# Performance work log

Hardware: AMD Instinct MI355X
Metric: run time of the kernel (lower is better)

Reference implementation:

```python
import jax, jax.numpy as jnp
import numpy as np


def _t2p(x):
    # [B, N, C] -> [B, C, H, H]
    B, N, C = x.shape
    H = int(round(N ** 0.5))
    return x.transpose(0, 2, 1).reshape(B, C, H, H)


def _p2t(x):
    # [B, C, H, W] -> [B, H*W, C]
    B, C, H, W = x.shape
    return x.reshape(B, C, H * W).transpose(0, 2, 1)


def _ln(x, g, b, eps=1e-5):
    m = jnp.mean(x, axis=-1, keepdims=True)
    v = jnp.var(x, axis=-1, keepdims=True)
    return (x - m) / jnp.sqrt(v + eps) * g + b


def _spectral(x, cw):
    # x: [B, C, H, W]; cw: [h, w//2+1, C, 2]
    y = x.transpose(0, 3, 2, 1).astype(jnp.float32)  # [B, W, H, C]
    a, b = y.shape[1], y.shape[2]
    f = jnp.fft.rfft2(y, axes=(1, 2), norm='ortho')   # [B, a, b//2+1, C]
    w = cw[..., 0] + 1j * cw[..., 1]
    y = jnp.fft.irfft2(f * w, s=(a, b), axes=(1, 2), norm='ortho')
    return y.transpose(0, 3, 2, 1)                    # [B, C, H, W]


def _branch(tok, cw, ln1_g, ln1_b, ln2_g, ln2_b, W1, b1, W2, b2):
    # tok: [B, N, 8]
    raw = tok
    t1 = _ln(_p2t(_t2p(tok)), ln1_g, ln1_b)
    p1 = _spectral(_t2p(t1), cw)
    t2 = _ln(_p2t(p1), ln2_g, ln2_b)
    h = jax.nn.gelu(t2 @ W1 + b1, approximate=False)  # exact GELU like torch default
    return (h @ W2 + b2) + raw


def setup_inputs() -> dict:
    key = jax.random.key(0)
    ks = jax.random.split(key, 16)
    B, N, D, HID = 256, 320, 768, 8
    inp = {
        'x': jax.random.normal(ks[0], (B, N, D), dtype=jnp.float32),
        'Wd': jax.random.normal(ks[1], (D, HID), dtype=jnp.float32) * 0.02,
        'bd': jax.random.normal(ks[2], (HID,), dtype=jnp.float32) * 0.02,
        'cw_x': jax.random.normal(ks[3], (16, 9, HID, 2), dtype=jnp.float32) * 0.02,
        'cw_z': jax.random.normal(ks[4], (8, 5, HID, 2), dtype=jnp.float32) * 0.02,
        'ln1_g': jnp.ones((HID,), dtype=jnp.float32),
        'ln1_b': jnp.zeros((HID,), dtype=jnp.float32),
        'ln2_g': jnp.ones((HID,), dtype=jnp.float32),
        'ln2_b': jnp.zeros((HID,), dtype=jnp.float32),
        'W1': jax.random.normal(ks[5], (HID, 2 * HID), dtype=jnp.float32) * 0.1,
        'b1': jnp.zeros((2 * HID,), dtype=jnp.float32),
        'W2': jax.random.normal(ks[6], (2 * HID, HID), dtype=jnp.float32) * 0.1,
        'b2': jnp.zeros((HID,), dtype=jnp.float32),
        'Wu': jax.random.normal(ks[7], (HID, D), dtype=jnp.float32) * 0.02,
        'bu': jnp.zeros((D,), dtype=jnp.float32),
    }
    return inp


def reference(x, Wd, bd, cw_x, cw_z, ln1_g, ln1_b, ln2_g, ln2_b, W1, b1, W2, b2, Wu, bu):
    h = x @ Wd + bd               # [B, 320, 8] adapter_down
    z = h[:, :64, :]              # 8x8 template tokens
    xx = h[:, 64:, :]             # 16x16 search tokens
    # NOTE: original code reuses norm_x1/norm_x2/mlp_x for both branches.
    xo = _branch(xx, cw_x, ln1_g, ln1_b, ln2_g, ln2_b, W1, b1, W2, b2)
    zo = _branch(z, cw_z, ln1_g, ln1_b, ln2_g, ln2_b, W1, b1, W2, b2)
    cat = jnp.concatenate([zo, xo], axis=1)  # [B, 320, 8]
    return cat @ Wu + bu          # adapter_up -> [B, 320, 768]
```

## Files before the change

kernel.cpp:

```cpp
#include <hip/hip_runtime.h>
#include <math.h>

#define PI_F 3.14159265358979323846f
#define SWZ16(i) ((i) ^ (((i) >> 4) & 7))
#define SWZ8(i)  ((i) ^ (((i) >> 3) & 7))

__global__ __launch_bounds__(256) void build_tables(
    const float* __restrict__ cw_x, const float* __restrict__ cw_z,
    float* __restrict__ KKx, float* __restrict__ KKz)
{
    int tid = blockIdx.x * 256 + threadIdx.x;
    if (tid < 2048) {
        int c = tid & 7;
        int ab = tid >> 3;
        int a = ab >> 4, b = ab & 15;
        float acc = 0.f;
        for (int u = 0; u < 16; ++u) {
            for (int v = 0; v < 9; ++v) {
                float m = (v == 0 || v == 8) ? 1.f : 2.f;
                int ph = (u * a + v * b) & 15;
                float th = (2.f * PI_F / 16.f) * (float)ph;
                float sn, cs;
                sincosf(th, &sn, &cs);
                const float* wp = cw_x + (size_t)((u * 9 + v) * 8 + c) * 2;
                acc += m * (wp[0] * cs - wp[1] * sn);
            }
        }
        KKx[ab * 8 + c] = acc * (1.f / 256.f);
    } else if (tid < 2048 + 512) {
        int e = tid - 2048;
        int c = e & 7;
        int ab = e >> 3;
        int a = ab >> 3, b = ab & 7;
        float acc = 0.f;
        for (int u = 0; u < 8; ++u) {
            for (int v = 0; v < 5; ++v) {
                float m = (v == 0 || v == 4) ? 1.f : 2.f;
                int ph = (u * a + v * b) & 7;
                float th = (2.f * PI_F / 8.f) * (float)ph;
                float sn, cs;
                sincosf(th, &sn, &cs);
                const float* wp = cw_z + (size_t)((u * 5 + v) * 8 + c) * 2;
                acc += m * (wp[0] * cs - wp[1] * sn);
            }
        }
        KKz[ab * 8 + c] = acc * (1.f / 64.f);
    }
}

__global__ __launch_bounds__(256) void down_proj(
    const float* __restrict__ x, const float* __restrict__ Wd,
    const float* __restrict__ bd, float* __restrict__ h)
{
    __shared__ float4 wds[1536];
    int t = threadIdx.x;
    const float4* Wd4 = (const float4*)Wd;
    #pragma unroll
    for (int j = 0; j < 6; ++j) {
        int i = t + 256 * j;
        wds[SWZ8(i)] = Wd4[i];
    }
    __syncthreads();

    int lane = t & 63;
    int wave = t >> 6;
    int sub  = lane >> 4;
    int l    = lane & 15;
    int row  = blockIdx.x * 16 + wave * 4 + sub;

    const float4* xr = (const float4*)x + (size_t)row * 192;
    float a0=0.f,a1=0.f,a2=0.f,a3=0.f,a4=0.f,a5=0.f,a6=0.f,a7=0.f;
    #pragma unroll
    for (int j = 0; j < 12; ++j) {
        float4 v = xr[l + 16 * j];
        int k0 = (l + 16 * j) * 4;
        float xv[4] = {v.x, v.y, v.z, v.w};
        #pragma unroll
        for (int e = 0; e < 4; ++e) {
            int f4 = (k0 + e) * 2;
            int sw = SWZ8(f4);
            float4 w0 = wds[sw];
            float4 w1 = wds[sw ^ 1];
            a0 += xv[e] * w0.x;  a1 += xv[e] * w0.y;
            a2 += xv[e] * w0.z;  a3 += xv[e] * w0.w;
            a4 += xv[e] * w1.x;  a5 += xv[e] * w1.y;
            a6 += xv[e] * w1.z;  a7 += xv[e] * w1.w;
        }
    }
    #pragma unroll
    for (int off = 1; off < 16; off <<= 1) {
        a0 += __shfl_xor(a0, off, 64);  a1 += __shfl_xor(a1, off, 64);
        a2 += __shfl_xor(a2, off, 64);  a3 += __shfl_xor(a3, off, 64);
        a4 += __shfl_xor(a4, off, 64);  a5 += __shfl_xor(a5, off, 64);
        a6 += __shfl_xor(a6, off, 64);  a7 += __shfl_xor(a7, off, 64);
    }
    if (l == 0) {
        float4* hp = (float4*)h + (size_t)row * 2;
        hp[0] = make_float4(a0 + bd[0], a1 + bd[1], a2 + bd[2], a3 + bd[3]);
        hp[1] = make_float4(a4 + bd[4], a5 + bd[5], a6 + bd[6], a7 + bd[7]);
    }
}

__global__ __launch_bounds__(256) void branch_kernel(
    const float* __restrict__ h,
    const float* __restrict__ KKx, const float* __restrict__ KKz,
    const float* __restrict__ g1v, const float* __restrict__ b1v,
    const float* __restrict__ g2v, const float* __restrict__ b2v,
    const float* __restrict__ W1, const float* __restrict__ b1m,
    const float* __restrict__ W2, const float* __restrict__ b2m,
    float* __restrict__ cat)
{
    __shared__ float4 t1s[512];
    __shared__ float4 kks[512];
    __shared__ float sW1[128], sW2[128], sB1[16], sB2[8];
    __shared__ float sG1[8], sH1[8], sG2[8], sH2[8];

    int t = threadIdx.x;
    int bid = blockIdx.x;
    bool isX = (bid >= 64);

    if (t < 128) { sW1[t] = W1[t]; sW2[t] = W2[t]; }
    if (t < 16)  sB1[t] = b1m[t];
    if (t < 8) { sB2[t] = b2m[t]; sG1[t] = g1v[t]; sH1[t] = b1v[t]; sG2[t] = g2v[t]; sH2[t] = b2v[t]; }

    int rowidx;
    if (isX) {
        rowidx = (bid - 64) * 320 + 64 + t;
    } else {
        int w = t >> 6, tz = t & 63;
        rowidx = (bid * 4 + w) * 320 + tz;
    }
    const float4* hp = (const float4*)h + (size_t)rowidx * 2;
    float4 r0 = hp[0], r1 = hp[1];

    if (isX) {
        const float4* K4 = (const float4*)KKx;
        kks[t] = K4[t];  kks[t + 256] = K4[t + 256];
    } else {
        if (t < 128) kks[t] = ((const float4*)KKz)[t];
    }
    __syncthreads();

    float raw[8] = {r0.x, r0.y, r0.z, r0.w, r1.x, r1.y, r1.z, r1.w};
    float mean = 0.f;
    #pragma unroll
    for (int c = 0; c < 8; ++c) mean += raw[c];
    mean *= 0.125f;
    float var = 0.f;
    #pragma unroll
    for (int c = 0; c < 8; ++c) { float d = raw[c] - mean; var += d * d; }
    var *= 0.125f;
    float inv = rsqrtf(var + 1e-5f);
    float t1[8];
    #pragma unroll
    for (int c = 0; c < 8; ++c) t1[c] = (raw[c] - mean) * inv * sG1[c] + sH1[c];

    int base, i0;
    if (isX) { base = 0; i0 = 2 * t; }
    else     { int w = t >> 6, tz = t & 63; base = w * 128; i0 = 2 * tz; }
    t1s[base + SWZ16(i0)]     = make_float4(t1[0], t1[1], t1[2], t1[3]);
    t1s[base + SWZ16(i0 + 1)] = make_float4(t1[4], t1[5], t1[6], t1[7]);
    __syncthreads();

    float s0=0.f,s1=0.f,s2=0.f,s3=0.f,s4=0.f,s5=0.f,s6=0.f,s7=0.f;
    if (isX) {
        int p = t >> 4, q = t & 15;
        for (int da = 0; da < 16; ++da) {
            int qp = (q - da) & 15;
            #pragma unroll
            for (int db = 0; db < 16; ++db) {
                int pp = (p - db) & 15;
                int si = (pp * 16 + qp) * 2;
                float4 v0 = t1s[SWZ16(si)];
                float4 v1 = t1s[SWZ16(si + 1)];
                int kb = (da * 16 + db) * 2;
                float4 k0 = kks[kb], k1 = kks[kb + 1];
                s0 += k0.x * v0.x;  s1 += k0.y * v0.y;
                s2 += k0.z * v0.z;  s3 += k0.w * v0.w;
                s4 += k1.x * v1.x;  s5 += k1.y * v1.y;
                s6 += k1.z * v1.z;  s7 += k1.w * v1.w;
            }
        }
    } else {
        int w = t >> 6, tz = t & 63;
        int p = tz >> 3, q = tz & 7;
        int tb = w * 128;
        for (int da = 0; da < 8; ++da) {
            int qp = (q - da) & 7;
            #pragma unroll
            for (int db = 0; db < 8; ++db) {
                int pp = (p - db) & 7;
                int si = (pp * 8 + qp) * 2;
                float4 v0 = t1s[tb + SWZ16(si)];
                float4 v1 = t1s[tb + SWZ16(si + 1)];
                int kb = (da * 8 + db) * 2;
                float4 k0 = kks[kb], k1 = kks[kb + 1];
                s0 += k0.x * v0.x;  s1 += k0.y * v0.y;
                s2 += k0.z * v0.z;  s3 += k0.w * v0.w;
                s4 += k1.x * v1.x;  s5 += k1.y * v1.y;
                s6 += k1.z * v1.z;  s7 += k1.w * v1.w;
            }
        }
    }

    float sarr[8] = {s0, s1, s2, s3, s4, s5, s6, s7};
    float m2 = 0.f;
    #pragma unroll
    for (int c = 0; c < 8; ++c) m2 += sarr[c];
    m2 *= 0.125f;
    float v2 = 0.f;
    #pragma unroll
    for (int c = 0; c < 8; ++c) { float d = sarr[c] - m2; v2 += d * d; }
    v2 *= 0.125f;
    float inv2 = rsqrtf(v2 + 1e-5f);
    float t2[8];
    #pragma unroll
    for (int c = 0; c < 8; ++c) t2[c] = (sarr[c] - m2) * inv2 * sG2[c] + sH2[c];

    float hm[16];
    #pragma unroll
    for (int j = 0; j < 16; ++j) {
        float acc = sB1[j];
        #pragma unroll
        for (int c = 0; c < 8; ++c) acc += t2[c] * sW1[c * 16 + j];
        hm[j] = 0.5f * acc * (1.f + erff(acc * 0.70710678118654752f));
    }
    float o[8];
    #pragma unroll
    for (int c = 0; c < 8; ++c) {
        float acc = sB2[c];
        #pragma unroll
        for (int j = 0; j < 16; ++j) acc += hm[j] * sW2[j * 8 + c];
        o[c] = acc + raw[c];
    }
    float4* cp = (float4*)cat + (size_t)rowidx * 2;
    cp[0] = make_float4(o[0], o[1], o[2], o[3]);
    cp[1] = make_float4(o[4], o[5], o[6], o[7]);
}

__global__ __launch_bounds__(192) void up_proj(
    const float* __restrict__ cat, const float* __restrict__ Wu,
    const float* __restrict__ bu, float* __restrict__ out)
{
    __shared__ float4 wus[1536];
    __shared__ float crow[128];
    int t = threadIdx.x;
    const float4* Wu4 = (const float4*)Wu;
    #pragma unroll
    for (int j = 0; j < 8; ++j) wus[t + 192 * j] = Wu4[t + 192 * j];
    int row0 = blockIdx.x * 16;
    if (t < 128) crow[t] = cat[(size_t)row0 * 8 + t];
    __syncthreads();

    float4 wr[8];
    #pragma unroll
    for (int c = 0; c < 8; ++c) wr[c] = wus[c * 192 + t];
    float4 bv = ((const float4*)bu)[t];

    float4* outp = (float4*)out + (size_t)row0 * 192 + t;
    #pragma unroll
    for (int r = 0; r < 16; ++r) {
        const float* cr = &crow[r * 8];
        float4 acc = bv;
        #pragma unroll
        for (int c = 0; c < 8; ++c) {
            float cv = cr[c];
            acc.x += cv * wr[c].x;  acc.y += cv * wr[c].y;
            acc.z += cv * wr[c].z;  acc.w += cv * wr[c].w;
        }
        outp[(size_t)r * 192] = acc;
    }
}

extern "C" void kernel_launch(void* const* d_in, const int* in_sizes, int n_in,
                              void* d_out, int out_size, void* d_ws, size_t ws_size,
                              hipStream_t stream)
{
    (void)in_sizes; (void)n_in; (void)out_size; (void)ws_size;
    const float* x    = (const float*)d_in[0];
    const float* Wd   = (const float*)d_in[1];
    const float* bd   = (const float*)d_in[2];
    const float* cw_x = (const float*)d_in[3];
    const float* cw_z = (const float*)d_in[4];
    const float* g1   = (const float*)d_in[5];
    const float* h1   = (const float*)d_in[6];
    const float* g2   = (const float*)d_in[7];
    const float* h2   = (const float*)d_in[8];
    const float* W1   = (const float*)d_in[9];
    const float* b1   = (const float*)d_in[10];
    const float* W2   = (const float*)d_in[11];
    const float* b2   = (const float*)d_in[12];
    const float* Wu   = (const float*)d_in[13];
    const float* bu   = (const float*)d_in[14];
    float* out = (float*)d_out;

    float* h   = (float*)d_ws;
    float* cat = h + 655360;
    float* KKx = cat + 655360;
    float* KKz = KKx + 2048;

    hipLaunchKernelGGL(build_tables, dim3(10), dim3(256), 0, stream, cw_x, cw_z, KKx, KKz);
    hipLaunchKernelGGL(down_proj,    dim3(5120), dim3(256), 0, stream, x, Wd, bd, h);
    hipLaunchKernelGGL(branch_kernel, dim3(320), dim3(256), 0, stream,
                       h, KKx, KKz, g1, h1, g2, h2, W1, b1, W2, b2, cat);
    hipLaunchKernelGGL(up_proj,      dim3(5120), dim3(192), 0, stream, cat, Wu, bu, out);
}
```

Measured before the change: 182.8 us.

## Register-block down projection over four rows and drop Wu LDS staging

Each 16-lane group in down_proj now computes four rows instead of one, so every Wd value read from LDS is reused across four x rows, and the grid shrinks fourfold. up_proj no longer copies all of Wu into shared memory per block; each thread loads its eight float4 weights straight from global memory, relying on cache hits. The branch kernel's LDS swizzle is widened to a 4-bit XOR and computes the swizzle once per float4 pair. The trade-offs are more registers per thread in down_proj (32 accumulators plus shuffles) and global weight loads in up_proj.

New measurement: 187.0 us. 1.02x slower.

```diff
diff --git a/kernel.cpp b/kernel.cpp
--- a/kernel.cpp
+++ b/kernel.cpp
@@ -2,7 +2,7 @@
 #include <math.h>
 
 #define PI_F 3.14159265358979323846f
-#define SWZ16(i) ((i) ^ (((i) >> 4) & 7))
+#define SWZ16(i) ((i) ^ (((i) >> 4) & 15))
 #define SWZ8(i)  ((i) ^ (((i) >> 3) & 7))
 
 __global__ __launch_bounds__(256) void build_tables(
@@ -62,42 +62,55 @@
     }
     __syncthreads();
 
-    int lane = t & 63;
-    int wave = t >> 6;
-    int sub  = lane >> 4;
-    int l    = lane & 15;
-    int row  = blockIdx.x * 16 + wave * 4 + sub;
-
-    const float4* xr = (const float4*)x + (size_t)row * 192;
-    float a0=0.f,a1=0.f,a2=0.f,a3=0.f,a4=0.f,a5=0.f,a6=0.f,a7=0.f;
+    int g = t >> 4;
+    int l = t & 15;
+    int row0 = blockIdx.x * 64 + g * 4;
+
+    const float4* xr = (const float4*)x + (size_t)row0 * 192;
+    float acc[4][8];
+    #pragma unroll
+    for (int r = 0; r < 4; ++r)
+        #pragma unroll
+        for (int c = 0; c < 8; ++c) acc[r][c] = 0.f;
+
     #pragma unroll
     for (int j = 0; j < 12; ++j) {
-        float4 v = xr[l + 16 * j];
-        int k0 = (l + 16 * j) * 4;
-        float xv[4] = {v.x, v.y, v.z, v.w};
+        float4 v[4];
+        #pragma unroll
+        for (int r = 0; r < 4; ++r) v[r] = xr[(size_t)r * 192 + l + 16 * j];
         #pragma unroll
         for (int e = 0; e < 4; ++e) {
-            int f4 = (k0 + e) * 2;
+            int f4 = ((l + 16 * j) * 4 + e) * 2;
             int sw = SWZ8(f4);
             float4 w0 = wds[sw];
             float4 w1 = wds[sw ^ 1];
-            a0 += xv[e] * w0.x;  a1 += xv[e] * w0.y;
-            a2 += xv[e] * w0.z;  a3 += xv[e] * w0.w;
-            a4 += xv[e] * w1.x;  a5 += xv[e] * w1.y;
-            a6 += xv[e] * w1.z;  a7 += xv[e] * w1.w;
-        }
-    }
-    #pragma unroll
-    for (int off = 1; off < 16; off <<= 1) {
-        a0 += __shfl_xor(a0, off, 64);  a1 += __shfl_xor(a1, off, 64);
-        a2 += __shfl_xor(a2, off, 64);  a3 += __shfl_xor(a3, off, 64);
-        a4 += __shfl_xor(a4, off, 64);  a5 += __shfl_xor(a5, off, 64);
-        a6 += __shfl_xor(a6, off, 64);  a7 += __shfl_xor(a7, off, 64);
-    }
-    if (l == 0) {
-        float4* hp = (float4*)h + (size_t)row * 2;
-        hp[0] = make_float4(a0 + bd[0], a1 + bd[1], a2 + bd[2], a3 + bd[3]);
-        hp[1] = make_float4(a4 + bd[4], a5 + bd[5], a6 + bd[6], a7 + bd[7]);
+            #pragma unroll
+            for (int r = 0; r < 4; ++r) {
+                float xv = (e == 0) ? v[r].x : (e == 1) ? v[r].y : (e == 2) ? v[r].z : v[r].w;
+                acc[r][0] += xv * w0.x;  acc[r][1] += xv * w0.y;
+                acc[r][2] += xv * w0.z;  acc[r][3] += xv * w0.w;
+                acc[r][4] += xv * w1.x;  acc[r][5] += xv * w1.y;
+                acc[r][6] += xv * w1.z;  acc[r][7] += xv * w1.w;
+            }
+        }
+    }
+    #pragma unroll
+    for (int off = 1; off < 16; off <<= 1)
+        #pragma unroll
+        for (int r = 0; r < 4; ++r)
+            #pragma unroll
+            for (int c = 0; c < 8; ++c)
+                acc[r][c] += __shfl_xor(acc[r][c], off, 64);
+
+    if (l < 4) {
+        float o[8];
+        #pragma unroll
+        for (int c = 0; c < 8; ++c)
+            o[c] = (l == 0) ? acc[0][c] : (l == 1) ? acc[1][c] : (l == 2) ? acc[2][c] : acc[3][c];
+        float4 b0 = ((const float4*)bd)[0], b1 = ((const float4*)bd)[1];
+        float4* hp = (float4*)h + (size_t)(row0 + l) * 2;
+        hp[0] = make_float4(o[0] + b0.x, o[1] + b0.y, o[2] + b0.z, o[3] + b0.w);
+        hp[1] = make_float4(o[4] + b1.x, o[5] + b1.y, o[6] + b1.z, o[7] + b1.w);
     }
 }
 
@@ -171,8 +184,9 @@
             for (int db = 0; db < 16; ++db) {
                 int pp = (p - db) & 15;
                 int si = (pp * 16 + qp) * 2;
-                float4 v0 = t1s[SWZ16(si)];
-                float4 v1 = t1s[SWZ16(si + 1)];
+                int sw = SWZ16(si);
+                float4 v0 = t1s[sw];
+                float4 v1 = t1s[sw ^ 1];
                 int kb = (da * 16 + db) * 2;
                 float4 k0 = kks[kb], k1 = kks[kb + 1];
                 s0 += k0.x * v0.x;  s1 += k0.y * v0.y;
@@ -191,8 +205,9 @@
             for (int db = 0; db < 8; ++db) {
                 int pp = (p - db) & 7;
                 int si = (pp * 8 + qp) * 2;
-                float4 v0 = t1s[tb + SWZ16(si)];
-                float4 v1 = t1s[tb + SWZ16(si + 1)];
+                int sw = SWZ16(si);
+                float4 v0 = t1s[tb + sw];
+                float4 v1 = t1s[tb + (sw ^ 1)];
                 int kb = (da * 8 + db) * 2;
                 float4 k0 = kks[kb], k1 = kks[kb + 1];
                 s0 += k0.x * v0.x;  s1 += k0.y * v0.y;
@@ -242,19 +257,16 @@
     const float* __restrict__ cat, const float* __restrict__ Wu,
     const float* __restrict__ bu, float* __restrict__ out)
 {
-    __shared__ float4 wus[1536];
     __shared__ float crow[128];
     int t = threadIdx.x;
-    const float4* Wu4 = (const float4*)Wu;
-    #pragma unroll
-    for (int j = 0; j < 8; ++j) wus[t + 192 * j] = Wu4[t + 192 * j];
     int row0 = blockIdx.x * 16;
     if (t < 128) crow[t] = cat[(size_t)row0 * 8 + t];
     __syncthreads();
 
+    const float4* Wu4 = (const float4*)Wu;
     float4 wr[8];
     #pragma unroll
-    for (int c = 0; c < 8; ++c) wr[c] = wus[c * 192 + t];
+    for (int c = 0; c < 8; ++c) wr[c] = Wu4[c * 192 + t];
     float4 bv = ((const float4*)bu)[t];
 
     float4* outp = (float4*)out + (size_t)row0 * 192 + t;
@@ -300,7 +312,7 @@
     float* KKz = KKx + 2048;
 
     hipLaunchKernelGGL(build_tables, dim3(10), dim3(256), 0, stream, cw_x, cw_z, KKx, KKz);
-    hipLaunchKernelGGL(down_proj,    dim3(5120), dim3(256), 0, stream, x, Wd, bd, h);
+    hipLaunchKernelGGL(down_proj,    dim3(1280), dim3(256), 0, stream, x, Wd, bd, h);
     hipLaunchKernelGGL(branch_kernel, dim3(320), dim3(256), 0, stream,
                        h, KKx, KKz, g1, h1, g2, h2, W1, b1, W2, b2, cat);
     hipLaunchKernelGGL(up_proj,      dim3(5120), dim3(192), 0, stream, cat, Wu, bu, out);
```
